# Kernel optimization log

Hardware: AMD Instinct MI355X
Metric: run time of the kernel (lower is better)

## Reference

```python
import jax, jax.numpy as jnp
import numpy as np

B, T, N, DIN, D = 8, 20, 1000, 64, 64


def setup_inputs() -> dict:
    key = jax.random.key(0)
    ks = jax.random.split(key, 10)
    stdv = 1.0 / np.sqrt(DIN + D)  # torch reset_param: uniform(-1/sqrt(in_size), ...)
    def gate_w(k):
        return jax.random.uniform(k, (N, DIN + D, D), jnp.float32, -stdv, stdv)
    x = jax.random.normal(ks[0], (B, T, N, DIN), jnp.float32)
    # xavier_normal_ for time_att.W [N, T, D]: fan_in=T*D, fan_out=N*D
    xav_std = np.sqrt(2.0 / (T * D + N * D)).astype(np.float32)
    Wt = jax.random.normal(ks[5], (N, T, D), jnp.float32) * xav_std
    return {
        "x": x,
        "Wi": gate_w(ks[1]), "bi": jnp.zeros((N, D), jnp.float32),
        "Wo": gate_w(ks[2]), "bo": jnp.zeros((N, D), jnp.float32),
        "Wf": gate_w(ks[3]), "bf": jnp.zeros((N, D), jnp.float32),
        "Wc": gate_w(ks[4]), "bc": jnp.zeros((N, D), jnp.float32),
        "Wt": Wt,
    }


def _lstm_att(x, Wi, bi, Wo, bo, Wf, bf, Wc, bc, Wt):
    b, t, n, din = x.shape
    d = Wi.shape[-1]

    def gate(xh, W, bias):
        # per-stock matmul: [b,n,din+d] x [n,din+d,d] -> [b,n,d]
        return jnp.einsum('bni,nio->bno', xh, W) + bias

    def step(carry, xt):
        h, c = carry  # [b,n,d]
        xh = jnp.concatenate([xt, h], axis=-1)
        it = jax.nn.sigmoid(gate(xh, Wi, bi))
        ot = jax.nn.sigmoid(gate(xh, Wo, bo))
        ft = jax.nn.sigmoid(gate(xh, Wf, bf))
        ch = jnp.tanh(gate(xh, Wc, bc))
        c2 = ft * c + it * ch
        h2 = ot * jnp.tanh(c2)
        return (h2, c2), h2

    h0 = jnp.zeros((b, n, d), x.dtype)
    c0 = jnp.zeros((b, n, d), x.dtype)
    xt_seq = jnp.swapaxes(x, 0, 1)  # [t,b,n,din]
    _, hs = jax.lax.scan(step, (h0, c0), xt_seq)
    h = jnp.swapaxes(hs, 0, 1)  # [b,t,n,d] (torch.stack dim=-3)

    # time attention
    h_bntd = jnp.swapaxes(h, 1, 2)  # [b,n,t,d]
    scores = jnp.sum(h_bntd * Wt, axis=-1)  # [b,n,t]
    att = jax.nn.softmax(scores, axis=-1)
    out = jnp.einsum('bnt,bntd->bnd', att, h_bntd)  # matmul([b,n,1,t],[b,n,t,d]).squeeze()
    return out  # [b,n,d]


def reference(x, Wi, bi, Wo, bo, Wf, bf, Wc, bc, Wt):
    return _lstm_att(x, Wi, bi, Wo, bo, Wf, bf, Wc, bc, Wt)
```

## Files before the change

kernel.cpp:

```cpp
#include <hip/hip_runtime.h>

#define TT 20
#define NSTK 1000
#define THREADS 256
#define XP 72

#define SC_SIG  1.44269504089f
#define SC_TANH 2.88539008178f

typedef float f32x4 __attribute__((ext_vector_type(4)));
typedef _Float16 f16x8 __attribute__((ext_vector_type(8)));
typedef _Float16 f16x2 __attribute__((ext_vector_type(2)));

__device__ __forceinline__ float rcp_f(float x) { return __builtin_amdgcn_rcpf(x); }
__device__ __forceinline__ float exp2_f(float x) { return __builtin_amdgcn_exp2f(x); }


extern "C" __global__ void __launch_bounds__(THREADS, 3)
lstm_att_lean(const float* __restrict__ x,
              const float* __restrict__ Wi, const float* __restrict__ bi,
              const float* __restrict__ Wo, const float* __restrict__ bo,
              const float* __restrict__ Wf, const float* __restrict__ bf_,
              const float* __restrict__ Wc, const float* __restrict__ bc,
              const float* __restrict__ Wt,
              float* __restrict__ out)
{
    __shared__ __align__(16) _Float16 xs[TT][8][XP];
    __shared__ __align__(16) _Float16 hh[TT + 1][8][XP];

    const int n    = blockIdx.x;
    const int tid  = threadIdx.x;
    const int lane = tid & 63;
    const int w    = tid >> 6;
    const int q    = lane >> 4;
    const int r16  = lane & 15;
    const int brow = r16 & 7;
    const int dcol = w * 16 + r16;
    const bool hi  = lane >= 32;
    const int rowbase = ((lane & 31) >> 4) * 4 + (hi ? 2 : 0);

    const int xrow = tid >> 5;
    const int xd   = (tid & 31) * 2;
    float2 xr[TT];
    #pragma unroll
    for (int u = 0; u < TT; ++u) {
        const int r = u * 8 + xrow;
        xr[u] = *(const float2*)(x + ((size_t)r * NSTK + n) * 64 + xd);
    }

    f16x8 bw[4][4];
    float biasv[4];
    {
        const float* Wg[4] = {Wi, Wo, Wf, Wc};
        const float* Bg[4] = {bi, bo, bf_, bc};
        #pragma unroll
        for (int g = 0; g < 4; ++g) {
            const float sc = (g == 3) ? SC_TANH : SC_SIG;
            const float* base = Wg[g] + (size_t)n * 8192 + dcol;
            #pragma unroll
            for (int kf = 0; kf < 4; ++kf)
                #pragma unroll
                for (int j = 0; j < 8; ++j)
                    bw[g][kf][j] = (_Float16)(base[(kf * 32 + q * 8 + j) * 64] * sc);
            biasv[g] = Bg[g][n * 64 + dcol] * sc;
        }
    }

    #pragma unroll
    for (int u = 0; u < TT; ++u) {
        const int r = u * 8 + xrow;
        const int b = r / TT, t = r % TT;
        *(f16x2*)(&xs[t][b][xd]) = (f16x2){(_Float16)xr[u].x, (_Float16)xr[u].y};
    }
    for (int i = tid; i < 8 * XP / 2; i += THREADS) ((unsigned*)hh)[i] = 0u;

    float cst0 = 0.f, cst1 = 0.f;
    __syncthreads();

    for (int t = 0; t < TT; ++t) {
        f16x8 af[4];
        af[0] = *(const f16x8*)(&xs[t][brow][q * 8]);
        af[1] = *(const f16x8*)(&xs[t][brow][32 + q * 8]);
        af[2] = *(const f16x8*)(&hh[t][brow][q * 8]);
        af[3] = *(const f16x8*)(&hh[t][brow][32 + q * 8]);

        f32x4 acc[4];
        #pragma unroll
        for (int g = 0; g < 4; ++g)
            acc[g] = (f32x4){biasv[g], biasv[g], biasv[g], biasv[g]};
        #pragma unroll
        for (int kf = 0; kf < 4; ++kf) {
            #pragma unroll
            for (int g = 0; g < 4; ++g)
                acc[g] = __builtin_amdgcn_mfma_f32_16x16x32_f16(af[kf], bw[g][kf], acc[g], 0, 0, 0);
        }

        float p0[4], p1[4];
        #pragma unroll
        for (int g = 0; g < 4; ++g) {
            const float t2 = __shfl_xor(acc[g][2], 32, 64);
            const float t3 = __shfl_xor(acc[g][3], 32, 64);
            p0[g] = hi ? t2 : acc[g][0];
            p1[g] = hi ? t3 : acc[g][1];
        }

        const float ig0 = rcp_f(1.0f + exp2_f(-p0[0]));
        const float og0 = rcp_f(1.0f + exp2_f(-p0[1]));
        const float fg0 = rcp_f(1.0f + exp2_f(-p0[2]));
        const float cg0 = 1.0f - 2.0f * rcp_f(exp2_f(p0[3]) + 1.0f);
        const float ig1 = rcp_f(1.0f + exp2_f(-p1[0]));
        const float og1 = rcp_f(1.0f + exp2_f(-p1[1]));
        const float fg1 = rcp_f(1.0f + exp2_f(-p1[2]));
        const float cg1 = 1.0f - 2.0f * rcp_f(exp2_f(p1[3]) + 1.0f);
        cst0 = fmaf(fg0, cst0, ig0 * cg0);
        cst1 = fmaf(fg1, cst1, ig1 * cg1);
        const float h0 = og0 * (1.0f - 2.0f * rcp_f(exp2_f(cst0 * SC_TANH) + 1.0f));
        const float h1 = og1 * (1.0f - 2.0f * rcp_f(exp2_f(cst1 * SC_TANH) + 1.0f));

        hh[t + 1][rowbase][dcol]     = (_Float16)h0;
        hh[t + 1][rowbase + 1][dcol] = (_Float16)h1;

        __syncthreads();
    }

    const float* wtg = Wt + (size_t)n * (TT * 64);
    #pragma unroll
    for (int bb = 0; bb < 2; ++bb) {
        const int b = 2 * w + bb;
        float s[TT];
        #pragma unroll
        for (int t = 0; t < TT; ++t)
            s[t] = (float)hh[t + 1][b][lane] * wtg[t * 64 + lane];
        #pragma unroll
        for (int t = 0; t < TT; ++t) {
            #pragma unroll
            for (int mk = 32; mk >= 1; mk >>= 1)
                s[t] += __shfl_xor(s[t], mk, 64);
        }
        float m = s[0];
        #pragma unroll
        for (int t = 1; t < TT; ++t) m = fmaxf(m, s[t]);
        float se = 0.f;
        #pragma unroll
        for (int t = 0; t < TT; ++t) { s[t] = exp2_f((s[t] - m) * SC_SIG); se += s[t]; }
        const float rs = rcp_f(se);
        float o = 0.f;
        #pragma unroll
        for (int t = 0; t < TT; ++t)
            o = fmaf(s[t], (float)hh[t + 1][b][lane], o);
        out[((size_t)b * NSTK + n) * 64 + lane] = o * rs;
    }
}

extern "C" void kernel_launch(void* const* d_in, const int* in_sizes, int n_in,
                              void* d_out, int out_size, void* d_ws, size_t ws_size,
                              hipStream_t stream) {
    const float* x  = (const float*)d_in[0];
    const float* Wi = (const float*)d_in[1];
    const float* bi = (const float*)d_in[2];
    const float* Wo = (const float*)d_in[3];
    const float* bo = (const float*)d_in[4];
    const float* Wf = (const float*)d_in[5];
    const float* bf = (const float*)d_in[6];
    const float* Wc = (const float*)d_in[7];
    const float* bc = (const float*)d_in[8];
    const float* Wt = (const float*)d_in[9];
    float* out = (float*)d_out;

    lstm_att_lean<<<NSTK, THREADS, 0, stream>>>(
        x, Wi, bi, Wo, bo, Wf, bf, Wc, bc, Wt, out);
}
```

Before: 68.81 us.

## Stream x per timestep through double-buffered LDS and raise occupancy bound

Instead of loading all 20 timesteps of x into registers and LDS up front, each step now prefetches the next timestep's x into a register and writes it to a two-slot LDS buffer, overlapping global loads with the MFMA recurrence. This shrinks the LDS footprint and register pressure, so the launch bound's waves-per-EU hint rises from 3 to 4. The trade-off is that global load latency now sits inside the serial time loop, which can stall steps if the prefetch distance is not enough.

```diff
diff --git a/kernel.cpp b/kernel.cpp
--- a/kernel.cpp
+++ b/kernel.cpp
@@ -3,7 +3,7 @@
 #define TT 20
 #define NSTK 1000
 #define THREADS 256
-#define XP 72
+#define HP 72
 
 #define SC_SIG  1.44269504089f
 #define SC_TANH 2.88539008178f
@@ -16,17 +16,17 @@
 __device__ __forceinline__ float exp2_f(float x) { return __builtin_amdgcn_exp2f(x); }
 
 
-extern "C" __global__ void __launch_bounds__(THREADS, 3)
-lstm_att_lean(const float* __restrict__ x,
-              const float* __restrict__ Wi, const float* __restrict__ bi,
-              const float* __restrict__ Wo, const float* __restrict__ bo,
-              const float* __restrict__ Wf, const float* __restrict__ bf_,
-              const float* __restrict__ Wc, const float* __restrict__ bc,
-              const float* __restrict__ Wt,
-              float* __restrict__ out)
+extern "C" __global__ void __launch_bounds__(THREADS, 4)
+lstm_att_v11(const float* __restrict__ x,
+             const float* __restrict__ Wi, const float* __restrict__ bi,
+             const float* __restrict__ Wo, const float* __restrict__ bo,
+             const float* __restrict__ Wf, const float* __restrict__ bf_,
+             const float* __restrict__ Wc, const float* __restrict__ bc,
+             const float* __restrict__ Wt,
+             float* __restrict__ out)
 {
-    __shared__ __align__(16) _Float16 xs[TT][8][XP];
-    __shared__ __align__(16) _Float16 hh[TT + 1][8][XP];
+    __shared__ __align__(16) _Float16 hh[TT + 1][8][HP];
+    __shared__ __align__(16) _Float16 xb[2][8][HP];
 
     const int n    = blockIdx.x;
     const int tid  = threadIdx.x;
@@ -38,15 +38,6 @@
     const int dcol = w * 16 + r16;
     const bool hi  = lane >= 32;
     const int rowbase = ((lane & 31) >> 4) * 4 + (hi ? 2 : 0);
-
-    const int xrow = tid >> 5;
-    const int xd   = (tid & 31) * 2;
-    float2 xr[TT];
-    #pragma unroll
-    for (int u = 0; u < TT; ++u) {
-        const int r = u * 8 + xrow;
-        xr[u] = *(const float2*)(x + ((size_t)r * NSTK + n) * 64 + xd);
-    }
 
     f16x8 bw[4][4];
     float biasv[4];
@@ -66,23 +57,34 @@
         }
     }
 
-    #pragma unroll
-    for (int u = 0; u < TT; ++u) {
-        const int r = u * 8 + xrow;
-        const int b = r / TT, t = r % TT;
-        *(f16x2*)(&xs[t][b][xd]) = (f16x2){(_Float16)xr[u].x, (_Float16)xr[u].y};
+    const int sb = tid >> 5, dx = (tid & 31) * 2;
+    const float* xptr = x + ((size_t)sb * TT * NSTK + (size_t)n) * 64 + dx;
+
+    {
+        const float2 x0 = *(const float2*)xptr;
+        *(f16x2*)(&xb[0][sb][dx]) = (f16x2){(_Float16)x0.x, (_Float16)x0.y};
     }
-    for (int i = tid; i < 8 * XP / 2; i += THREADS) ((unsigned*)hh)[i] = 0u;
+    for (int i = tid; i < 8 * HP / 2; i += THREADS) ((unsigned*)hh)[i] = 0u;
+    float2 xreg = *(const float2*)(xptr + (size_t)NSTK * 64);
 
     float cst0 = 0.f, cst1 = 0.f;
     __syncthreads();
 
     for (int t = 0; t < TT; ++t) {
+        const int cur = t & 1, nxt = cur ^ 1;
+
         f16x8 af[4];
-        af[0] = *(const f16x8*)(&xs[t][brow][q * 8]);
-        af[1] = *(const f16x8*)(&xs[t][brow][32 + q * 8]);
+        af[0] = *(const f16x8*)(&xb[cur][brow][q * 8]);
+        af[1] = *(const f16x8*)(&xb[cur][brow][32 + q * 8]);
         af[2] = *(const f16x8*)(&hh[t][brow][q * 8]);
         af[3] = *(const f16x8*)(&hh[t][brow][32 + q * 8]);
+
+        if (t + 1 < TT)
+            *(f16x2*)(&xb[nxt][sb][dx]) = (f16x2){(_Float16)xreg.x, (_Float16)xreg.y};
+        {
+            const size_t off = (size_t)((t + 2 < TT) ? t + 2 : TT - 1) * (NSTK * 64);
+            xreg = *(const float2*)(xptr + off);
+        }
 
         f32x4 acc[4];
         #pragma unroll
@@ -167,6 +169,6 @@
     const float* Wt = (const float*)d_in[9];
     float* out = (float*)d_out;
 
-    lstm_att_lean<<<NSTK, THREADS, 0, stream>>>(
+    lstm_att_v11<<<NSTK, THREADS, 0, stream>>>(
         x, Wi, bi, Wo, bo, Wf, bf, Wc, bc, Wt, out);
 }
```

Result: faster. 65.02 us (-5.5%).
